# Kernel optimization log

Measured on AMD Instinct MI355X. Metric: run time of the kernel, lower is better.

## Reference

```python
import jax, jax.numpy as jnp
import numpy as np
from jax import lax

B, T = 8192, 4096


def setup_inputs() -> dict:
    key = jax.random.key(0)
    ks = jax.random.split(key, 16)
    P = jax.random.uniform(ks[0], (B, T, 1), dtype=jnp.float32) * 10.0  # precipitation, mm
    lengths = jax.random.randint(ks[1], (B,), 1, T + 1, dtype=jnp.int32)
    initial_S = jax.random.uniform(ks[2], (4,), dtype=jnp.float32) * 20.0  # initial tank levels
    Area = jnp.array([100.0], dtype=jnp.float32)  # catchment area km^2
    baseflow = jnp.array([0.0], dtype=jnp.float32)  # unused by forward, kept for signature fidelity

    def u(k, lo, hi):
        return jax.random.uniform(k, (1,), dtype=jnp.float32) * (hi - lo) + lo

    params = {
        "outflow_rate_1_h1": u(ks[3], 0.05, 0.25),
        "outflow_rate_1_h2": u(ks[4], 0.05, 0.10),
        "height_1_h1": u(ks[5], 40.0, 60.0),
        "height_1_h2": u(ks[6], 0.0, 40.0),
        "inflow_rate_2": u(ks[7], 0.01, 0.30),
        "outflow_rate_2": u(ks[8], 0.005, 0.30),
        "height_2": u(ks[9], 0.0, 30.0),
        "inflow_rate_3": u(ks[10], 0.005, 0.20),
        "outflow_rate_3": u(ks[11], 0.005, 0.15),
        "height_3": u(ks[12], 0.0, 30.0),
        "inflow_rate_4": u(ks[13], 0.005, 0.10),
        "outflow_rate_4": u(ks[14], 0.0006, 0.10),
    }
    return {"P": P, "lengths": lengths, "initial_S": initial_S, "Area": Area,
            "baseflow": baseflow, **params}


def reference(P, lengths, initial_S, Area, baseflow,
              outflow_rate_1_h1, outflow_rate_1_h2, height_1_h1, height_1_h2,
              inflow_rate_2, outflow_rate_2, height_2,
              inflow_rate_3, outflow_rate_3, height_3,
              inflow_rate_4, outflow_rate_4):
    Pq = P[..., 0]                              # [B, T]
    b, t = Pq.shape
    # valid_mask[b, t] = (lengths[b] > t), as in pad_packed_sequence masking
    mask = (jnp.arange(t)[None, :] < lengths[:, None]).astype(Pq.dtype)  # [B, T]
    w_init = tuple(jnp.broadcast_to(initial_S[i], (b,)) for i in range(4))

    def step(carry, xs):
        w1, w2, w3, w4 = carry
        p, m = xs                               # [B] each
        # Tank 1: two side outlets + bottom percolation into tank 2
        of1h1 = jnp.maximum(outflow_rate_1_h1 * (w1 - height_1_h1 + p), 0.0) * m
        of1h2 = jnp.maximum(outflow_rate_1_h2 * (w1 - height_1_h2 + p), 0.0) * m
        of1 = (of1h1 + of1h2) * m
        out12 = jnp.maximum(inflow_rate_2 * (w1 + p), 0.0) * m
        w1 = w1 + (p - of1 - out12) * m
        # Tank 2
        of2 = jnp.maximum(outflow_rate_2 * (w2 + out12 - height_2), 0.0) * m
        out23 = jnp.maximum(inflow_rate_3 * (w2 + out12), 0.0) * m
        w2 = w2 + (out12 - of2 - out23) * m
        # Tank 3
        of3 = jnp.maximum(outflow_rate_3 * (w3 + out23 - height_3), 0.0) * m
        out34 = jnp.maximum(inflow_rate_4 * (w3 + out23), 0.0) * m
        w3 = w3 + (out23 - of3 - out34) * m
        # Tank 4 (deep baseflow tank)
        of4 = jnp.maximum(outflow_rate_4 * (w4 + out34), 0.0) * m
        w4 = w4 + (out34 - of4) * m
        total = (of1 + of2 + of3 + of4) * m
        return (w1, w2, w3, w4), total * Area / 3.6   # mm -> m^3/s conversion

    _, ys = lax.scan(step, w_init, (Pq.T, mask.T))    # ys: [T, B]
    return ys.T                                        # [B, T]
```

## Files before the change

kernel.cpp:

```cpp
#include <hip/hip_runtime.h>
#include <stdint.h>


__device__ __forceinline__ float quad_rot1(float x) {
    int xi = __builtin_bit_cast(int, x);
    int r = __builtin_amdgcn_update_dpp(xi, xi, 0x93, 0xF, 0xF, false);
    return __builtin_bit_cast(float, r);
}

__global__ __launch_bounds__(64)
void tank_kernel(
    const float* __restrict__ P,
    const int*   __restrict__ lengths,
    const float* __restrict__ S0,
    const float* __restrict__ AreaP,
    const float* __restrict__ p_r1h1, const float* __restrict__ p_r1h2,
    const float* __restrict__ p_h1h1, const float* __restrict__ p_h1h2,
    const float* __restrict__ p_ri2,  const float* __restrict__ p_ro2,
    const float* __restrict__ p_h2,
    const float* __restrict__ p_ri3,  const float* __restrict__ p_ro3,
    const float* __restrict__ p_h3,
    const float* __restrict__ p_ri4,  const float* __restrict__ p_ro4,
    float* __restrict__ Out,
    int B, int T)
{
    __shared__ float4 inbuf[2 * 256];
    __shared__ float4 outbuf[3 * 256];

    const int tid = threadIdx.x;
    const int g   = tid >> 2;
    const int k   = tid & 3;
    const int row = blockIdx.x * 16 + g;
    const int rowc = (row < B) ? row : (B - 1);
    const bool is3 = (k == 3);
    const float zk = (k == 0) ? 0.0f : 1.0f;

    const float v_r1h1 = p_r1h1[0], v_r1h2 = p_r1h2[0];
    const float v_h11 = p_h1h1[0], v_h12 = p_h1h2[0];
    const float v_ri2 = p_ri2[0], v_ro2 = p_ro2[0], v_h2 = p_h2[0];
    const float v_ri3 = p_ri3[0], v_ro3 = p_ro3[0], v_h3 = p_h3[0];
    const float v_ri4 = p_ri4[0], v_ro4 = p_ro4[0];
    const float scale = AreaP[0] * (1.0f / 3.6f);

    float rA = v_ro4, kA = 0.0f, rB = 0.0f, kB = 0.0f, riN = 0.0f;
    if (k == 0) { rA = v_r1h1; kA = -v_r1h1 * v_h11; rB = v_r1h2; kB = -v_r1h2 * v_h12; riN = v_ri2; }
    else if (k == 1) { rA = v_ro2; kA = -v_ro2 * v_h2; riN = v_ri3; }
    else if (k == 2) { rA = v_ro3; kA = -v_ro3 * v_h3; riN = v_ri4; }

    float w = (k == 0) ? S0[0] : (k == 1) ? S0[1] : (k == 2) ? S0[2] : S0[3];

    int len = lengths[rowc];
    if (len > T) len = T;
    if (len < 0) len = 0;

    float psum = 0.0f;
    float hand = 0.0f;
    float4 o = make_float4(0.0f, 0.0f, 0.0f, 0.0f);
    const int ntiles = T / 64;

#define STEP(HANDC, ii, ocomp) do {                          \
        float in_   = quad_rot1(hand);                       \
        float prin_ = quad_rot1(psum);                       \
        float t_  = w + in_;                                 \
        float a1_ = fmaxf(fmaf(rA, t_, kA), 0.0f);           \
        float a2_ = fmaxf(fmaf(rB, t_, kB), 0.0f);           \
        float e3_ = fmaxf(t_, 0.0f);                         \
        float fl_ = riN * e3_;                               \
        float Y_  = a1_ + a2_;                               \
        w = (t_ - fl_) - Y_;                                 \
        psum = fmaf(prin_, zk, Y_);                          \
        hand = is3 ? (HANDC) : fl_;                          \
        (ocomp) = psum;                                      \
    } while (0)

#define STEPW(HANDC, ii, ocomp) do {                         \
        float in_   = quad_rot1(hand);                       \
        float prin_ = quad_rot1(psum);                       \
        float t_  = w + in_;                                 \
        float a1_ = fmaxf(fmaf(rA, t_, kA), 0.0f);           \
        float a2_ = fmaxf(fmaf(rB, t_, kB), 0.0f);           \
        float e3_ = fmaxf(t_, 0.0f);                         \
        float fl_ = riN * e3_;                               \
        float Y_  = a1_ + a2_;                               \
        float wn_ = (t_ - fl_) - Y_;                         \
        w = ((ii) >= k) ? wn_ : w;                           \
        psum = fmaf(prin_, zk, Y_);                          \
        hand = is3 ? (HANDC) : fl_;                          \
        (ocomp) = psum;                                      \
    } while (0)

#define STAGE_LOAD(mt) do {                                               \
        const float* src_ = P + (size_t)rowc * T + (mt) * 64;             \
        _Pragma("unroll")                                                 \
        for (int r = 0; r < 4; ++r)                                       \
            st[r] = *reinterpret_cast<const float4*>(src_ + (4 * r + k) * 4); \
    } while (0)

#define STAGE_LDS(ibp) do {                                  \
        _Pragma("unroll")                                    \
        for (int r = 0; r < 4; ++r)                          \
            (ibp)[g * 16 + ((4 * r + k) ^ g)] = st[r];       \
    } while (0)

#define OUT_STORE(mt) do {                                                \
        const float4* ob_ = outbuf + ((mt) % 3) * 256;                    \
        const int col0_ = (mt) * 64;                                      \
        _Pragma("unroll")                                                 \
        for (int r = 0; r < 4; ++r) {                                     \
            float4 v_ = ob_[g * 16 + ((4 * r + k) ^ g)];                  \
            const int cb_ = col0_ + (4 * r + k) * 4;                      \
            float4 s_;                                                    \
            s_.x = (cb_ + 0 < len) ? v_.x * scale : 0.0f;                 \
            s_.y = (cb_ + 1 < len) ? v_.y * scale : 0.0f;                 \
            s_.z = (cb_ + 2 < len) ? v_.z * scale : 0.0f;                 \
            s_.w = (cb_ + 3 < len) ? v_.w * scale : 0.0f;                 \
            if (row < B)                                                  \
                *reinterpret_cast<float4*>(Out + (size_t)row * T + cb_) = s_; \
        }                                                                 \
    } while (0)

#define TILE_BODY(STEPM, GUARD0, i0v, ibp) do {                           \
        float4 c0 = (ibp)[g * 16 + (0 ^ g)];                              \
        float4 c1 = (ibp)[g * 16 + (1 ^ g)];                              \
        float4 c2 = (ibp)[g * 16 + (2 ^ g)];                              \
        hand = is3 ? c0.x : hand;                                         \
        _Pragma("unroll 4")                                               \
        for (int j4 = 0; j4 < 16; ++j4) {                                 \
            float4 c3 = (ibp)[g * 16 + ((((j4 + 3) & 15)) ^ g)];          \
            const int i_ = (i0v) + 4 * j4;                                \
            STEPM(c0.y, i_ + 0, o.y);                                     \
            STEPM(c0.z, i_ + 1, o.z);                                     \
            STEPM(c0.w, i_ + 2, o.w);                                     \
            const int b_ = ((i0v) >> 2) + j4 - 1;                         \
            if ((!(GUARD0) || b_ >= 0) && is3) {                          \
                float4* obp_ = outbuf + ((b_ >> 4) % 3) * 256;            \
                obp_[g * 16 + ((b_ & 15) ^ g)] = o;                       \
            }                                                             \
            STEPM(c1.x, i_ + 3, o.x);                                     \
            c0 = c1; c1 = c2; c2 = c3;                                    \
        }                                                                 \
    } while (0)

    float4 st[4];
    STAGE_LOAD(0);
    STAGE_LDS(inbuf);
    __syncthreads();
    if (ntiles > 1) STAGE_LOAD(1);
    TILE_BODY(STEPW, 1, 0, inbuf);

    for (int m = 1; m < ntiles; ++m) {
        float4* ib = inbuf + (m & 1) * 256;
        STAGE_LDS(ib);
        __syncthreads();
        if (m >= 2) OUT_STORE(m - 2);
        if (m + 1 < ntiles) STAGE_LOAD(m + 1);
        TILE_BODY(STEP, 0, m * 64, ib);
    }

    STEP(0.0f, 0, o.y);
    STEP(0.0f, 0, o.z);
    STEP(0.0f, 0, o.w);
    {
        const int lastb = (T >> 2) - 1;
        if (is3) {
            float4* obp = outbuf + ((lastb >> 4) % 3) * 256;
            obp[g * 16 + ((lastb & 15) ^ g)] = o;
        }
    }
#undef STEP
#undef STEPW
#undef TILE_BODY

    __syncthreads();
    OUT_STORE(ntiles - 2);
    OUT_STORE(ntiles - 1);
#undef OUT_STORE
#undef STAGE_LOAD
#undef STAGE_LDS
}

extern "C" void kernel_launch(void* const* d_in, const int* in_sizes, int n_in,
                              void* d_out, int out_size, void* d_ws, size_t ws_size,
                              hipStream_t stream) {
    const float* P        = (const float*)d_in[0];
    const int*   lengths  = (const int*)d_in[1];
    const float* S0       = (const float*)d_in[2];
    const float* Area     = (const float*)d_in[3];
    const float* r1h1 = (const float*)d_in[5];
    const float* r1h2 = (const float*)d_in[6];
    const float* h1h1 = (const float*)d_in[7];
    const float* h1h2 = (const float*)d_in[8];
    const float* ri2  = (const float*)d_in[9];
    const float* ro2  = (const float*)d_in[10];
    const float* h2   = (const float*)d_in[11];
    const float* ri3  = (const float*)d_in[12];
    const float* ro3  = (const float*)d_in[13];
    const float* h3   = (const float*)d_in[14];
    const float* ri4  = (const float*)d_in[15];
    const float* ro4  = (const float*)d_in[16];
    float* out = (float*)d_out;

    const int B = in_sizes[1];
    const int T = in_sizes[0] / B;

    dim3 block(64);
    dim3 grid((B + 15) / 16);
    hipLaunchKernelGGL(tank_kernel, grid, block, 0, stream,
                       P, lengths, S0, Area,
                       r1h1, r1h2, h1h1, h1h2,
                       ri2, ro2, h2, ri3, ro3, h3, ri4, ro4,
                       out, B, T);
}
```

Baseline: 456.4 us.

## Batch four timesteps per quad-lane hop to cut DPP shuffle dependency chains

The wavefront pipeline previously passed one value at a time between the four tank lanes, so every timestep needed two DPP rotates on the serial path. Each lane now carries four independent flux and partial-sum registers, and a hop advances four timesteps per rotate batch. Tank 0 consumes whole float4 precipitation chunks, and the pipeline skew becomes three hops rather than three steps. This raises register use and adds a longer drain epilogue, in exchange for more instruction-level parallelism and fewer cross-lane waits per step.

```diff
diff --git a/kernel.cpp b/kernel.cpp
--- a/kernel.cpp
+++ b/kernel.cpp
@@ -32,6 +32,7 @@
     const int k   = tid & 3;
     const int row = blockIdx.x * 16 + g;
     const int rowc = (row < B) ? row : (B - 1);
+    const bool is0 = (k == 0);
     const bool is3 = (k == 3);
     const float zk = (k == 0) ? 0.0f : 1.0f;
 
@@ -53,40 +54,64 @@
     if (len > T) len = T;
     if (len < 0) len = 0;
 
-    float psum = 0.0f;
-    float hand = 0.0f;
-    float4 o = make_float4(0.0f, 0.0f, 0.0f, 0.0f);
+    float fl0 = 0.0f, fl1 = 0.0f, fl2 = 0.0f, fl3 = 0.0f;
+    float ps0 = 0.0f, ps1 = 0.0f, ps2 = 0.0f, ps3 = 0.0f;
     const int ntiles = T / 64;
 
-#define STEP(HANDC, ii, ocomp) do {                          \
-        float in_   = quad_rot1(hand);                       \
-        float prin_ = quad_rot1(psum);                       \
-        float t_  = w + in_;                                 \
-        float a1_ = fmaxf(fmaf(rA, t_, kA), 0.0f);           \
-        float a2_ = fmaxf(fmaf(rB, t_, kB), 0.0f);           \
-        float e3_ = fmaxf(t_, 0.0f);                         \
-        float fl_ = riN * e3_;                               \
-        float Y_  = a1_ + a2_;                               \
-        w = (t_ - fl_) - Y_;                                 \
-        psum = fmaf(prin_, zk, Y_);                          \
-        hand = is3 ? (HANDC) : fl_;                          \
-        (ocomp) = psum;                                      \
-    } while (0)
-
-#define STEPW(HANDC, ii, ocomp) do {                         \
-        float in_   = quad_rot1(hand);                       \
-        float prin_ = quad_rot1(psum);                       \
-        float t_  = w + in_;                                 \
-        float a1_ = fmaxf(fmaf(rA, t_, kA), 0.0f);           \
-        float a2_ = fmaxf(fmaf(rB, t_, kB), 0.0f);           \
-        float e3_ = fmaxf(t_, 0.0f);                         \
-        float fl_ = riN * e3_;                               \
-        float Y_  = a1_ + a2_;                               \
-        float wn_ = (t_ - fl_) - Y_;                         \
-        w = ((ii) >= k) ? wn_ : w;                           \
-        psum = fmaf(prin_, zk, Y_);                          \
-        hand = is3 ? (HANDC) : fl_;                          \
-        (ocomp) = psum;                                      \
+#define HOP4(CX, CY, CZ, CW, FREEZE, hidx) do {                   \
+        float r0_ = quad_rot1(fl0);                               \
+        float r1_ = quad_rot1(fl1);                               \
+        float r2_ = quad_rot1(fl2);                               \
+        float r3_ = quad_rot1(fl3);                               \
+        float q0_ = quad_rot1(ps0);                               \
+        float q1_ = quad_rot1(ps1);                               \
+        float q2_ = quad_rot1(ps2);                               \
+        float q3_ = quad_rot1(ps3);                               \
+        float i0_ = is0 ? (CX) : r0_;                             \
+        float i1_ = is0 ? (CY) : r1_;                             \
+        float i2_ = is0 ? (CZ) : r2_;                             \
+        float i3_ = is0 ? (CW) : r3_;                             \
+        float t_, a1_, a2_, e_, Y_, wn_;                          \
+                                                      \
+        t_  = w + i0_;                                            \
+        a1_ = fmaxf(fmaf(rA, t_, kA), 0.0f);                      \
+        a2_ = fmaxf(fmaf(rB, t_, kB), 0.0f);                      \
+        e_  = fmaxf(t_, 0.0f);                                    \
+        fl0 = riN * e_;                                           \
+        Y_  = a1_ + a2_;                                          \
+        wn_ = (t_ - fl0) - Y_;                                    \
+        w = (FREEZE) ? (((hidx) >= k) ? wn_ : w) : wn_;           \
+        ps0 = fmaf(q0_, zk, Y_);                                  \
+                                                      \
+        t_  = w + i1_;                                            \
+        a1_ = fmaxf(fmaf(rA, t_, kA), 0.0f);                      \
+        a2_ = fmaxf(fmaf(rB, t_, kB), 0.0f);                      \
+        e_  = fmaxf(t_, 0.0f);                                    \
+        fl1 = riN * e_;                                           \
+        Y_  = a1_ + a2_;                                          \
+        wn_ = (t_ - fl1) - Y_;                                    \
+        w = (FREEZE) ? (((hidx) >= k) ? wn_ : w) : wn_;           \
+        ps1 = fmaf(q1_, zk, Y_);                                  \
+                                                      \
+        t_  = w + i2_;                                            \
+        a1_ = fmaxf(fmaf(rA, t_, kA), 0.0f);                      \
+        a2_ = fmaxf(fmaf(rB, t_, kB), 0.0f);                      \
+        e_  = fmaxf(t_, 0.0f);                                    \
+        fl2 = riN * e_;                                           \
+        Y_  = a1_ + a2_;                                          \
+        wn_ = (t_ - fl2) - Y_;                                    \
+        w = (FREEZE) ? (((hidx) >= k) ? wn_ : w) : wn_;           \
+        ps2 = fmaf(q2_, zk, Y_);                                  \
+                                                      \
+        t_  = w + i3_;                                            \
+        a1_ = fmaxf(fmaf(rA, t_, kA), 0.0f);                      \
+        a2_ = fmaxf(fmaf(rB, t_, kB), 0.0f);                      \
+        e_  = fmaxf(t_, 0.0f);                                    \
+        fl3 = riN * e_;                                           \
+        Y_  = a1_ + a2_;                                          \
+        wn_ = (t_ - fl3) - Y_;                                    \
+        w = (FREEZE) ? (((hidx) >= k) ? wn_ : w) : wn_;           \
+        ps3 = fmaf(q3_, zk, Y_);                                  \
     } while (0)
 
 #define STAGE_LOAD(mt) do {                                               \
@@ -119,25 +144,20 @@
         }                                                                 \
     } while (0)
 
-#define TILE_BODY(STEPM, GUARD0, i0v, ibp) do {                           \
+#define TILE_BODY(FREEZE, h0, ibp) do {                                   \
         float4 c0 = (ibp)[g * 16 + (0 ^ g)];                              \
         float4 c1 = (ibp)[g * 16 + (1 ^ g)];                              \
-        float4 c2 = (ibp)[g * 16 + (2 ^ g)];                              \
-        hand = is3 ? c0.x : hand;                                         \
         _Pragma("unroll 4")                                               \
         for (int j4 = 0; j4 < 16; ++j4) {                                 \
-            float4 c3 = (ibp)[g * 16 + ((((j4 + 3) & 15)) ^ g)];          \
-            const int i_ = (i0v) + 4 * j4;                                \
-            STEPM(c0.y, i_ + 0, o.y);                                     \
-            STEPM(c0.z, i_ + 1, o.z);                                     \
-            STEPM(c0.w, i_ + 2, o.w);                                     \
-            const int b_ = ((i0v) >> 2) + j4 - 1;                         \
-            if ((!(GUARD0) || b_ >= 0) && is3) {                          \
+            float4 c2 = (ibp)[g * 16 + (((j4 + 2) & 15) ^ g)];            \
+            HOP4(c0.x, c0.y, c0.z, c0.w, FREEZE, j4);                     \
+            const int b_ = (h0) + j4 - 3;                                 \
+            if ((!(FREEZE) || b_ >= 0) && is3) {                          \
                 float4* obp_ = outbuf + ((b_ >> 4) % 3) * 256;            \
-                obp_[g * 16 + ((b_ & 15) ^ g)] = o;                       \
+                obp_[g * 16 + ((b_ & 15) ^ g)] =                          \
+                    make_float4(ps0, ps1, ps2, ps3);                      \
             }                                                             \
-            STEPM(c1.x, i_ + 3, o.x);                                     \
-            c0 = c1; c1 = c2; c2 = c3;                                    \
+            c0 = c1; c1 = c2;                                             \
         }                                                                 \
     } while (0)
 
@@ -146,7 +166,7 @@
     STAGE_LDS(inbuf);
     __syncthreads();
     if (ntiles > 1) STAGE_LOAD(1);
-    TILE_BODY(STEPW, 1, 0, inbuf);
+    TILE_BODY(1, 0, inbuf);
 
     for (int m = 1; m < ntiles; ++m) {
         float4* ib = inbuf + (m & 1) * 256;
@@ -154,21 +174,22 @@
         __syncthreads();
         if (m >= 2) OUT_STORE(m - 2);
         if (m + 1 < ntiles) STAGE_LOAD(m + 1);
-        TILE_BODY(STEP, 0, m * 64, ib);
+        TILE_BODY(0, m * 16, ib);
     }
 
-    STEP(0.0f, 0, o.y);
-    STEP(0.0f, 0, o.z);
-    STEP(0.0f, 0, o.w);
     {
-        const int lastb = (T >> 2) - 1;
-        if (is3) {
-            float4* obp = outbuf + ((lastb >> 4) % 3) * 256;
-            obp[g * 16 + ((lastb & 15) ^ g)] = o;
+        const int nb = T >> 2;
+        #pragma unroll
+        for (int d = 0; d < 3; ++d) {
+            HOP4(0.0f, 0.0f, 0.0f, 0.0f, 0, 0);
+            const int b_ = nb - 3 + d;
+            if (is3) {
+                float4* obp = outbuf + ((b_ >> 4) % 3) * 256;
+                obp[g * 16 + ((b_ & 15) ^ g)] = make_float4(ps0, ps1, ps2, ps3);
+            }
         }
     }
-#undef STEP
-#undef STEPW
+#undef HOP4
 #undef TILE_BODY
 
     __syncthreads();
```

New measurement: 439.7 us. 1.04x faster.
